# Kernel tuning notes

Hardware: AMD Instinct MI355X
Metric: run time of the kernel (lower is better)

## Reference

```python
import jax, jax.numpy as jnp
import numpy as np

B, S, D, H = 2, 2048, 1024, 16
HD = D // H

def setup_inputs() -> dict:
    key = jax.random.key(0)
    ks = jax.random.split(key, 5)
    scale = 1.0 / np.sqrt(D)
    x = jax.random.normal(ks[0], (B, S, D), dtype=jnp.float32)
    W_qkv = jax.random.normal(ks[1], (D, 3 * D), dtype=jnp.float32) * scale
    b_qkv = jnp.zeros((3 * D,), dtype=jnp.float32)
    W_proj = jax.random.normal(ks[2], (D, D), dtype=jnp.float32) * scale
    b_proj = jnp.zeros((D,), dtype=jnp.float32)
    return {"x": x, "W_qkv": W_qkv, "b_qkv": b_qkv, "W_proj": W_proj, "b_proj": b_proj}

def reference(x, W_qkv, b_qkv, W_proj, b_proj):
    # qkv projection: [B,S,3D]
    qkv = jnp.einsum('bsd,df->bsf', x, W_qkv) + b_qkv
    q, k, v = jnp.split(qkv, 3, axis=-1)
    # reshape to heads: [B,H,S,hd]
    q = q.reshape(B, S, H, HD).transpose(0, 2, 1, 3)
    k = k.reshape(B, S, H, HD).transpose(0, 2, 1, 3)
    v = v.reshape(B, S, H, HD).transpose(0, 2, 1, 3)
    scores = jnp.einsum('bhqd,bhkd->bhqk', q, k) / jnp.sqrt(jnp.float32(HD))
    attn = jax.nn.softmax(scores, axis=-1)
    out = jnp.einsum('bhqk,bhkd->bhqd', attn, v)
    out = out.transpose(0, 2, 1, 3).reshape(B, S, D)
    return jnp.einsum('bsd,df->bsf', out, W_proj) + b_proj
```

## Files before the change

### kernel.cpp

```cpp
#include <hip/hip_runtime.h>

#define BATCH 2
#define SLEN 2048
#define DMODEL 1024
#define NHEAD 16
#define HDIM 64
#define MROWS (BATCH * SLEN)

typedef __attribute__((ext_vector_type(8))) short bf16x8;
typedef __attribute__((ext_vector_type(4))) short bf16x4;
typedef __attribute__((ext_vector_type(4))) float f32x4;
typedef __attribute__((ext_vector_type(8))) _Float16 f16x8;
typedef __attribute__((ext_vector_type(4))) _Float16 f16x4;

__device__ inline short f2bf(float x) {
    union { float f; unsigned u; } v; v.f = x;
    unsigned r = (v.u + 0x7FFFu + ((v.u >> 16) & 1u)) >> 16;
    return (short)r;
}
__device__ inline float bf2f(short h) {
    union { unsigned u; float f; } v; v.u = ((unsigned)(unsigned short)h) << 16;
    return v.f;
}
__device__ inline unsigned fbits(float x) {
    union { float f; unsigned u; } v; v.f = x; return v.u;
}
__device__ inline float hw_exp2(float x) {
    float r;
    asm("v_exp_f32 %0, %1" : "=v"(r) : "v"(x));
    return r;
}

__global__ __launch_bounds__(256) void cast_f16(
    const float* __restrict__ in, _Float16* __restrict__ out, int n4)
{
    int i = blockIdx.x * 256 + threadIdx.x;
    if (i >= n4) return;
    float4 f = ((const float4*)in)[i];
    f16x4 h;
    h[0] = (_Float16)f.x; h[1] = (_Float16)f.y;
    h[2] = (_Float16)f.z; h[3] = (_Float16)f.w;
    ((f16x4*)out)[i] = h;
}

__global__ __launch_bounds__(256) void transpose_f16(
    const float* __restrict__ in, _Float16* __restrict__ outT, int K, int N)
{
    __shared__ float T[64][68];
    const int tid = threadIdx.x;
    const int n0 = blockIdx.x * 64, k0 = blockIdx.y * 64;
#pragma unroll
    for (int i = 0; i < 4; i++) {
        int idx = tid + i * 256;
        int r = idx >> 4, c4 = idx & 15;
        *(float4*)&T[r][c4 * 4] = *(const float4*)&in[(size_t)(k0 + r) * N + n0 + c4 * 4];
    }
    __syncthreads();
#pragma unroll
    for (int i = 0; i < 4; i++) {
        int idx = tid + i * 256;
        int n = idx >> 4, kg = idx & 15;
        f16x4 h;
#pragma unroll
        for (int j = 0; j < 4; j++)
            h[j] = (_Float16)T[kg * 4 + j][n];
        *(f16x4*)&outT[(size_t)(n0 + n) * K + k0 + kg * 4] = h;
    }
}

__global__ __launch_bounds__(256) void transpose_v(
    const short* __restrict__ qkv, short* __restrict__ vT)
{
    __shared__ short T[64 * 68];
    const int tid = threadIdx.x;
    const int bid = blockIdx.x;
    const int st = bid & 31, h = (bid >> 5) & 15, b = bid >> 9;
    const int s0 = st * 64;
    const short* src = qkv + (size_t)b * SLEN * (3 * DMODEL) + 2 * DMODEL + h * HDIM;

    const int srow = tid >> 3, sc8 = tid & 7;
#pragma unroll
    for (int it = 0; it < 2; it++) {
        int s = srow + it * 32;
        *(bf16x8*)&T[s * 68 + sc8 * 8] =
            *(const bf16x8*)&src[(size_t)(s0 + s) * (3 * DMODEL) + sc8 * 8];
    }
    __syncthreads();

    const int d = tid >> 2, sq = tid & 3;
    short* dst = vT + ((size_t)(b * NHEAD + h) * HDIM + d) * SLEN + s0 + sq * 16;
    bf16x8 o0, o1;
#pragma unroll
    for (int j = 0; j < 8; j++) {
        o0[j] = T[(sq * 16 + j) * 68 + d];
        o1[j] = T[(sq * 16 + 8 + j) * 68 + d];
    }
    *(bf16x8*)&dst[0] = o0;
    *(bf16x8*)&dst[8] = o1;
}

#define GSTR 40

template<int OUT_BF16>
__global__ __launch_bounds__(256) void gemm_f16(
    const _Float16* __restrict__ A, const _Float16* __restrict__ Bw,
    const float* __restrict__ bias, void* __restrict__ Cout,
    int M, int N, int K)
{
    __shared__ _Float16 As[128 * GSTR], Bs[128 * GSTR];

    const int tid  = threadIdx.x;
    const int wave = tid >> 6, lane = tid & 63;
    const int quad = lane >> 4, lr = lane & 15;
    const int wm = (wave >> 1) * 64, wn = (wave & 1) * 64;
    const int row0 = blockIdx.y * 128, col0 = blockIdx.x * 128;

    f32x4 acc[4][4];
#pragma unroll
    for (int i = 0; i < 4; i++)
#pragma unroll
        for (int j = 0; j < 4; j++) acc[i][j] = (f32x4){0.f, 0.f, 0.f, 0.f};

    const int sr = tid >> 2, sc = tid & 3;

    for (int k0 = 0; k0 < K; k0 += 32) {
        __syncthreads();
#pragma unroll
        for (int i = 0; i < 2; i++) {
            int rr = sr + i * 64;
            size_t ga = (size_t)(row0 + rr) * K + k0 + sc * 8;
            size_t gb = (size_t)(col0 + rr) * K + k0 + sc * 8;
            int ls = rr * GSTR + sc * 8;
            *(f16x8*)&As[ls] = *(const f16x8*)&A[ga];
            *(f16x8*)&Bs[ls] = *(const f16x8*)&Bw[gb];
        }
        __syncthreads();

        f16x8 af[4];
#pragma unroll
        for (int mt = 0; mt < 4; mt++)
            af[mt] = *(const f16x8*)&As[(wm + mt * 16 + lr) * GSTR + quad * 8];
#pragma unroll
        for (int nt = 0; nt < 4; nt++) {
            f16x8 b = *(const f16x8*)&Bs[(wn + nt * 16 + lr) * GSTR + quad * 8];
#pragma unroll
            for (int mt = 0; mt < 4; mt++)
                acc[mt][nt] = __builtin_amdgcn_mfma_f32_16x16x32_f16(af[mt], b, acc[mt][nt], 0, 0, 0);
        }
    }

#pragma unroll
    for (int mt = 0; mt < 4; mt++) {
#pragma unroll
        for (int nt = 0; nt < 4; nt++) {
            int col = col0 + wn + nt * 16 + lr;
            float bv = bias[col];
#pragma unroll
            for (int r = 0; r < 4; r++) {
                int row = row0 + wm + mt * 16 + quad * 4 + r;
                float v = acc[mt][nt][r] + bv;
                if (OUT_BF16)
                    ((short*)Cout)[(size_t)row * N + col] = f2bf(v);
                else
                    ((float*)Cout)[(size_t)row * N + col] = v;
            }
        }
    }
}

#define ASTR 76
#define NT   (SLEN / 64)
#define QK_SCALE_LOG2E 0.1803368801111244f

__global__ __launch_bounds__(256) void attn_mfma(
    const short* __restrict__ qkv, const short* __restrict__ vT,
    _Float16* __restrict__ attn)
{
    __shared__ short Ks[2][64 * ASTR];
    __shared__ short Vt[2][64 * ASTR];

    const int tid  = threadIdx.x;
    const int lane = tid & 63;
    const int wave = tid >> 6;
    const int quad = lane >> 4;
    const int lr   = lane & 15;
    const int wq0  = wave * 16;

    const int bid = blockIdx.x;
    const int qt = bid & 31;
    const int h  = (bid >> 5) & 15;
    const int b  = bid >> 9;
    const int q0 = qt * 64;

    const short* qbase = qkv + (size_t)b * SLEN * (3 * DMODEL) + h * HDIM;
    const short* kbase = qbase + DMODEL;
    const short* vtbase = vT + (size_t)(b * NHEAD + h) * HDIM * SLEN;

    bf16x8 qf[2];
#pragma unroll
    for (int ds2 = 0; ds2 < 2; ds2++) {
        bf16x8 q = *(const bf16x8*)&qbase[(size_t)(q0 + wq0 + lr) * (3 * DMODEL) + ds2 * 32 + quad * 8];
#pragma unroll
        for (int j = 0; j < 8; j++)
            q[j] = f2bf(bf2f(q[j]) * QK_SCALE_LOG2E);
        qf[ds2] = q;
    }

    bf16x4 ones;
#pragma unroll
    for (int j = 0; j < 4; j++) ones[j] = (short)0x3F80;

    f32x4 oacc[4];
#pragma unroll
    for (int t = 0; t < 4; t++) oacc[t] = (f32x4){0.f, 0.f, 0.f, 0.f};
    f32x4 sacc = {0.f, 0.f, 0.f, 0.f};

    const int srow = tid >> 3, sc8 = tid & 7;

    const short* kp0 = kbase + (size_t)srow * (3 * DMODEL) + sc8 * 8;
    const short* kp1 = kp0 + 32 * (3 * DMODEL);
    const short* vp0 = vtbase + (size_t)srow * SLEN + sc8 * 8;
    const short* vp1 = vp0 + 32 * SLEN;

    bf16x8 kpre[2], vpre[2];
    kpre[0] = *(const bf16x8*)kp0; kpre[1] = *(const bf16x8*)kp1;
    vpre[0] = *(const bf16x8*)vp0; vpre[1] = *(const bf16x8*)vp1;
    kp0 += 64 * (3 * DMODEL); kp1 += 64 * (3 * DMODEL);
    vp0 += 64; vp1 += 64;

    for (int kt = 0; kt < NT; kt++) {
        const int cur = kt & 1;
        short* ks = Ks[cur];
        short* vt = Vt[cur];

        *(bf16x8*)&ks[srow * ASTR + sc8 * 8] = kpre[0];
        *(bf16x8*)&ks[(srow + 32) * ASTR + sc8 * 8] = kpre[1];
        *(bf16x8*)&vt[srow * ASTR + sc8 * 8] = vpre[0];
        *(bf16x8*)&vt[(srow + 32) * ASTR + sc8 * 8] = vpre[1];

        if (kt + 1 < NT) {
            kpre[0] = *(const bf16x8*)kp0; kpre[1] = *(const bf16x8*)kp1;
            vpre[0] = *(const bf16x8*)vp0; vpre[1] = *(const bf16x8*)vp1;
            kp0 += 64 * (3 * DMODEL); kp1 += 64 * (3 * DMODEL);
            vp0 += 64; vp1 += 64;
        }

        __syncthreads();

#pragma unroll
        for (int ct = 0; ct < 4; ct++) {
            const int krow = (ct * 16 + lr) * ASTR;
            bf16x4 k0a = *(const bf16x4*)&ks[krow + quad * 8];
            bf16x4 k0b = *(const bf16x4*)&ks[krow + quad * 8 + 4];
            bf16x4 k1a = *(const bf16x4*)&ks[krow + 32 + quad * 8];
            bf16x4 k1b = *(const bf16x4*)&ks[krow + 32 + quad * 8 + 4];
            bf16x8 kf0 = __builtin_shufflevector(k0a, k0b, 0, 1, 2, 3, 4, 5, 6, 7);
            bf16x8 kf1 = __builtin_shufflevector(k1a, k1b, 0, 1, 2, 3, 4, 5, 6, 7);

            f32x4 st = {0.f, 0.f, 0.f, 0.f};
            st = __builtin_amdgcn_mfma_f32_16x16x32_bf16(kf0, qf[0], st, 0, 0, 0);
            st = __builtin_amdgcn_mfma_f32_16x16x32_bf16(kf1, qf[1], st, 0, 0, 0);

            float p0[4];
#pragma unroll
            for (int r = 0; r < 4; r++) p0[r] = hw_exp2(st[r]);
            union { uint2 u; bf16x4 v; } pk0;
            pk0.u.x = __builtin_amdgcn_perm(fbits(p0[1]), fbits(p0[0]), 0x07060302u);
            pk0.u.y = __builtin_amdgcn_perm(fbits(p0[3]), fbits(p0[2]), 0x07060302u);
            bf16x4 pf0 = pk0.v;

            sacc = __builtin_amdgcn_mfma_f32_16x16x16bf16_1k(ones, pf0, sacc, 0, 0, 0);
#pragma unroll
            for (int dt = 0; dt < 4; dt++) {
                bf16x4 vf = *(const bf16x4*)&vt[(dt * 16 + lr) * ASTR + ct * 16 + quad * 4];
                oacc[dt] = __builtin_amdgcn_mfma_f32_16x16x16bf16_1k(vf, pf0, oacc[dt], 0, 0, 0);
            }
        }
    }

    {
        const float inv = 1.0f / sacc[0];
        const int row = b * SLEN + q0 + wq0 + lr;
#pragma unroll
        for (int dt = 0; dt < 4; dt++) {
            f16x4 h4;
#pragma unroll
            for (int r = 0; r < 4; r++)
                h4[r] = (_Float16)(oacc[dt][r] * inv);
            int col = h * HDIM + dt * 16 + quad * 4;
            *(f16x4*)&attn[(size_t)row * DMODEL + col] = h4;
        }
    }
}

extern "C" void kernel_launch(void* const* d_in, const int* in_sizes, int n_in,
                              void* d_out, int out_size, void* d_ws, size_t ws_size,
                              hipStream_t stream) {
    (void)in_sizes; (void)n_in; (void)out_size; (void)ws_size;
    const float* x     = (const float*)d_in[0];
    const float* Wqkv  = (const float*)d_in[1];
    const float* bqkv  = (const float*)d_in[2];
    const float* Wproj = (const float*)d_in[3];
    const float* bproj = (const float*)d_in[4];
    float* out = (float*)d_out;

    short* qkv = (short*)d_ws;
    _Float16* xf = (_Float16*)(qkv + (size_t)MROWS * 3 * DMODEL);
    _Float16* wq = xf + (size_t)MROWS * DMODEL;
    _Float16* wp = wq + (size_t)3 * DMODEL * DMODEL;
    short* vT = (short*)(wp + (size_t)DMODEL * DMODEL);
    _Float16* attnb = (_Float16*)(vT + (size_t)MROWS * DMODEL);

    cast_f16<<<dim3(MROWS * DMODEL / 4 / 256), 256, 0, stream>>>(x, xf, MROWS * DMODEL / 4);
    transpose_f16<<<dim3(3 * DMODEL / 64, DMODEL / 64), 256, 0, stream>>>(Wqkv, wq, DMODEL, 3 * DMODEL);
    transpose_f16<<<dim3(DMODEL / 64, DMODEL / 64), 256, 0, stream>>>(Wproj, wp, DMODEL, DMODEL);

    gemm_f16<1><<<dim3(3 * DMODEL / 128, MROWS / 128), 256, 0, stream>>>(
        xf, wq, bqkv, (void*)qkv, MROWS, 3 * DMODEL, DMODEL);

    transpose_v<<<dim3(BATCH * NHEAD * (SLEN / 64)), 256, 0, stream>>>(qkv, vT);

    attn_mfma<<<dim3(BATCH * NHEAD * (SLEN / 64)), 256, 0, stream>>>(qkv, vT, attnb);

    gemm_f16<0><<<dim3(DMODEL / 128, MROWS / 128), 256, 0, stream>>>(
        attnb, wp, bproj, (void*)out, MROWS, DMODEL, DMODEL);
}
```

Before: 234.6 us.

## Split attention key tiles across waves and reduce partial outputs in shared memory

Each wave used to own 16 query rows and loop over all 64 keys of every tile. Now each wave owns a 16-key slice of the tile and computes all 64 query rows, so every K and V fragment is loaded from LDS once per tile rather than four times. Because softmax uses no running max, the per-wave partial numerators and denominators can be summed directly, which happens at the end through a shared-memory reduction. The cost is four times more accumulator registers (which may lower occupancy or cause spills) and an epilogue with extra barriers.

```diff
diff --git a/kernel.cpp b/kernel.cpp
--- a/kernel.cpp
+++ b/kernel.cpp
@@ -170,21 +170,22 @@
 
 #define ASTR 76
 #define NT   (SLEN / 64)
+#define RSTR 20
 #define QK_SCALE_LOG2E 0.1803368801111244f
 
 __global__ __launch_bounds__(256) void attn_mfma(
     const short* __restrict__ qkv, const short* __restrict__ vT,
     _Float16* __restrict__ attn)
 {
-    __shared__ short Ks[2][64 * ASTR];
-    __shared__ short Vt[2][64 * ASTR];
+    __shared__ __align__(16) char smem[2 * 64 * ASTR * 2 * 2];
+    short* KsBuf = (short*)smem;
+    short* VtBuf = (short*)(smem + 2 * 64 * ASTR * 2);
 
     const int tid  = threadIdx.x;
     const int lane = tid & 63;
     const int wave = tid >> 6;
     const int quad = lane >> 4;
     const int lr   = lane & 15;
-    const int wq0  = wave * 16;
 
     const int bid = blockIdx.x;
     const int qt = bid & 31;
@@ -196,24 +197,30 @@
     const short* kbase = qbase + DMODEL;
     const short* vtbase = vT + (size_t)(b * NHEAD + h) * HDIM * SLEN;
 
-    bf16x8 qf[2];
-#pragma unroll
-    for (int ds2 = 0; ds2 < 2; ds2++) {
-        bf16x8 q = *(const bf16x8*)&qbase[(size_t)(q0 + wq0 + lr) * (3 * DMODEL) + ds2 * 32 + quad * 8];
-#pragma unroll
-        for (int j = 0; j < 8; j++)
-            q[j] = f2bf(bf2f(q[j]) * QK_SCALE_LOG2E);
-        qf[ds2] = q;
-    }
+    bf16x8 qf[4][2];
+#pragma unroll
+    for (int qs = 0; qs < 4; qs++)
+#pragma unroll
+        for (int ds2 = 0; ds2 < 2; ds2++) {
+            bf16x8 q = *(const bf16x8*)&qbase[(size_t)(q0 + qs * 16 + lr) * (3 * DMODEL) + ds2 * 32 + quad * 8];
+#pragma unroll
+            for (int j = 0; j < 8; j++)
+                q[j] = f2bf(bf2f(q[j]) * QK_SCALE_LOG2E);
+            qf[qs][ds2] = q;
+        }
 
     bf16x4 ones;
 #pragma unroll
     for (int j = 0; j < 4; j++) ones[j] = (short)0x3F80;
 
-    f32x4 oacc[4];
-#pragma unroll
-    for (int t = 0; t < 4; t++) oacc[t] = (f32x4){0.f, 0.f, 0.f, 0.f};
-    f32x4 sacc = {0.f, 0.f, 0.f, 0.f};
+    f32x4 oacc[4][4];
+#pragma unroll
+    for (int qs = 0; qs < 4; qs++)
+#pragma unroll
+        for (int t = 0; t < 4; t++) oacc[qs][t] = (f32x4){0.f, 0.f, 0.f, 0.f};
+    f32x4 sacc[4];
+#pragma unroll
+    for (int qs = 0; qs < 4; qs++) sacc[qs] = (f32x4){0.f, 0.f, 0.f, 0.f};
 
     const int srow = tid >> 3, sc8 = tid & 7;
 
@@ -228,10 +235,13 @@
     kp0 += 64 * (3 * DMODEL); kp1 += 64 * (3 * DMODEL);
     vp0 += 64; vp1 += 64;
 
+    const int krow = (wave * 16 + lr) * ASTR;
+    const int vcol = wave * 16 + quad * 4;
+
     for (int kt = 0; kt < NT; kt++) {
         const int cur = kt & 1;
-        short* ks = Ks[cur];
-        short* vt = Vt[cur];
+        short* ks = KsBuf + cur * 64 * ASTR;
+        short* vt = VtBuf + cur * 64 * ASTR;
 
         *(bf16x8*)&ks[srow * ASTR + sc8 * 8] = kpre[0];
         *(bf16x8*)&ks[(srow + 32) * ASTR + sc8 * 8] = kpre[1];
@@ -247,19 +257,23 @@
 
         __syncthreads();
 
-#pragma unroll
-        for (int ct = 0; ct < 4; ct++) {
-            const int krow = (ct * 16 + lr) * ASTR;
-            bf16x4 k0a = *(const bf16x4*)&ks[krow + quad * 8];
-            bf16x4 k0b = *(const bf16x4*)&ks[krow + quad * 8 + 4];
-            bf16x4 k1a = *(const bf16x4*)&ks[krow + 32 + quad * 8];
-            bf16x4 k1b = *(const bf16x4*)&ks[krow + 32 + quad * 8 + 4];
-            bf16x8 kf0 = __builtin_shufflevector(k0a, k0b, 0, 1, 2, 3, 4, 5, 6, 7);
-            bf16x8 kf1 = __builtin_shufflevector(k1a, k1b, 0, 1, 2, 3, 4, 5, 6, 7);
-
+        bf16x4 k0a = *(const bf16x4*)&ks[krow + quad * 8];
+        bf16x4 k0b = *(const bf16x4*)&ks[krow + quad * 8 + 4];
+        bf16x4 k1a = *(const bf16x4*)&ks[krow + 32 + quad * 8];
+        bf16x4 k1b = *(const bf16x4*)&ks[krow + 32 + quad * 8 + 4];
+        bf16x8 kf0 = __builtin_shufflevector(k0a, k0b, 0, 1, 2, 3, 4, 5, 6, 7);
+        bf16x8 kf1 = __builtin_shufflevector(k1a, k1b, 0, 1, 2, 3, 4, 5, 6, 7);
+
+        bf16x4 vf[4];
+#pragma unroll
+        for (int dt = 0; dt < 4; dt++)
+            vf[dt] = *(const bf16x4*)&vt[(dt * 16 + lr) * ASTR + vcol];
+
+#pragma unroll
+        for (int qs = 0; qs < 4; qs++) {
             f32x4 st = {0.f, 0.f, 0.f, 0.f};
-            st = __builtin_amdgcn_mfma_f32_16x16x32_bf16(kf0, qf[0], st, 0, 0, 0);
-            st = __builtin_amdgcn_mfma_f32_16x16x32_bf16(kf1, qf[1], st, 0, 0, 0);
+            st = __builtin_amdgcn_mfma_f32_16x16x32_bf16(kf0, qf[qs][0], st, 0, 0, 0);
+            st = __builtin_amdgcn_mfma_f32_16x16x32_bf16(kf1, qf[qs][1], st, 0, 0, 0);
 
             float p0[4];
 #pragma unroll
@@ -269,27 +283,50 @@
             pk0.u.y = __builtin_amdgcn_perm(fbits(p0[3]), fbits(p0[2]), 0x07060302u);
             bf16x4 pf0 = pk0.v;
 
-            sacc = __builtin_amdgcn_mfma_f32_16x16x16bf16_1k(ones, pf0, sacc, 0, 0, 0);
+            sacc[qs] = __builtin_amdgcn_mfma_f32_16x16x16bf16_1k(ones, pf0, sacc[qs], 0, 0, 0);
+#pragma unroll
+            for (int dt = 0; dt < 4; dt++)
+                oacc[qs][dt] = __builtin_amdgcn_mfma_f32_16x16x16bf16_1k(vf[dt], pf0, oacc[qs][dt], 0, 0, 0);
+        }
+    }
+
+    __syncthreads();
+    float* Lf = (float*)smem;
+    float* myrow = Lf + (wave * 64 + lane) * RSTR;
+
+#pragma unroll 1
+    for (int qs = 0; qs < 4; qs++) {
+#pragma unroll
+        for (int dt = 0; dt < 4; dt++)
+            *(f32x4*)&myrow[dt * 4] = oacc[qs][dt];
+        myrow[16] = sacc[qs][0];
+        __syncthreads();
+        if (wave == qs) {
+            f32x4 o[4];
+#pragma unroll
+            for (int dt = 0; dt < 4; dt++) o[dt] = (f32x4){0.f, 0.f, 0.f, 0.f};
+            float s = 0.f;
+#pragma unroll
+            for (int w = 0; w < 4; w++) {
+                const float* r2 = Lf + (w * 64 + lane) * RSTR;
+#pragma unroll
+                for (int dt = 0; dt < 4; dt++)
+                    o[dt] += *(const f32x4*)&r2[dt * 4];
+                s += r2[16];
+            }
+            const float inv = 1.0f / s;
+            const int row = b * SLEN + q0 + qs * 16 + lr;
 #pragma unroll
             for (int dt = 0; dt < 4; dt++) {
-                bf16x4 vf = *(const bf16x4*)&vt[(dt * 16 + lr) * ASTR + ct * 16 + quad * 4];
-                oacc[dt] = __builtin_amdgcn_mfma_f32_16x16x16bf16_1k(vf, pf0, oacc[dt], 0, 0, 0);
+                f16x4 h4;
+#pragma unroll
+                for (int r = 0; r < 4; r++)
+                    h4[r] = (_Float16)(o[dt][r] * inv);
+                int col = h * HDIM + dt * 16 + quad * 4;
+                *(f16x4*)&attn[(size_t)row * DMODEL + col] = h4;
             }
         }
-    }
-
-    {
-        const float inv = 1.0f / sacc[0];
-        const int row = b * SLEN + q0 + wq0 + lr;
-#pragma unroll
-        for (int dt = 0; dt < 4; dt++) {
-            f16x4 h4;
-#pragma unroll
-            for (int r = 0; r < 4; r++)
-                h4[r] = (_Float16)(oacc[dt][r] * inv);
-            int col = h * HDIM + dt * 16 + quad * 4;
-            *(f16x4*)&attn[(size_t)row * DMODEL + col] = h4;
-        }
+        __syncthreads();
     }
 }
 
```

After: 465.4 us. 1.98x slower.
